# Performance work log

Hardware: AMD Instinct MI355X
Metric: run time of the kernel (lower is better)

## Reference

```python
import jax, jax.numpy as jnp
import numpy as np
from jax import lax

R = 4                      # search_range
FILTERS = [128, 128, 96, 64, 32, 2]
B, H, W, C = 8, 128, 128, 128
IN_CH = (2 * R + 1) ** 2 + C + 2   # 81 + 128 + 2 = 211


def mish(x):
    return x * jnp.tanh(jax.nn.softplus(x))


def sepconv(x, dw, pw, b=None, act=True):
    # depthwise 3x3 (SAME) then pointwise 1x1, matching SeparableConv2D
    cin = x.shape[-1]
    y = lax.conv_general_dilated(
        x, dw, window_strides=(1, 1), padding='SAME',
        dimension_numbers=('NHWC', 'HWIO', 'NHWC'),
        feature_group_count=cin)
    y = jnp.einsum('bhwc,co->bhwo', y, pw)
    if b is not None:
        y = y + b
    return mish(y) if act else y


def warp(img, flo):
    # bilinear backward warp; TF casts float->int32 with truncation, jnp matches
    b_, h, w, _ = img.shape
    xs = jnp.arange(w, dtype=jnp.float32)[None, None, :]
    ys = jnp.arange(h, dtype=jnp.float32)[None, :, None]
    x = xs + flo[..., 0]
    y = ys + flo[..., 1]
    x0 = x.astype(jnp.int32)
    y0 = y.astype(jnp.int32)
    x1 = x0 + 1
    y1 = y0 + 1
    x0c = jnp.clip(x0, 0, w - 1)
    x1c = jnp.clip(x1, 0, w - 1)
    y0c = jnp.clip(y0, 0, h - 1)
    y1c = jnp.clip(y1, 0, h - 1)
    bi = jnp.arange(b_)[:, None, None]
    Ia = img[bi, y0c, x0c]
    Ib = img[bi, y1c, x0c]
    Ic = img[bi, y0c, x1c]
    Id = img[bi, y1c, x1c]
    x0f = x0c.astype(jnp.float32); x1f = x1c.astype(jnp.float32)
    y0f = y0c.astype(jnp.float32); y1f = y1c.astype(jnp.float32)
    wa = ((x1f - x) * (y1f - y))[..., None]
    wb = ((x1f - x) * (y - y0f))[..., None]
    wc = ((x - x0f) * (y1f - y))[..., None]
    wd = ((x - x0f) * (y - y0f))[..., None]
    return wa * Ia + wb * Ib + wc * Ic + wd * Id


def cost_volume(prv, nxt):
    _, h, w, _ = prv.shape
    d = 2 * R + 1
    pad = jnp.pad(nxt, ((0, 0), (R, R), (R, R), (0, 0)))
    costs = [jnp.mean(prv * pad[:, i:i + h, j:j + w, :], axis=-1)
             for i in range(d) for j in range(d)]
    return jnp.stack(costs, axis=-1)  # [B,H,W,81]


def setup_inputs() -> dict:
    key = jax.random.key(0)
    ks = iter(jax.random.split(key, 64))
    inp = {
        'prv': jax.random.normal(next(ks), (B, H, W, C), dtype=jnp.float32),
        'nxt': jax.random.normal(next(ks), (B, H, W, C), dtype=jnp.float32),
        'flo': jax.random.normal(next(ks), (B, H, W, 2), dtype=jnp.float32),
    }
    cin = IN_CH
    for i, f in enumerate(FILTERS):
        inp[f'dw{i}'] = 0.05 * jax.random.normal(next(ks), (3, 3, 1, cin), dtype=jnp.float32)
        inp[f'pw{i}'] = 0.05 * jax.random.normal(next(ks), (cin, f), dtype=jnp.float32)
        if i < len(FILTERS) - 1:
            inp[f'b{i}'] = 0.05 * jax.random.normal(next(ks), (f,), dtype=jnp.float32)
        cin = f
    return inp


def reference(prv, nxt, flo,
              dw0, pw0, b0, dw1, pw1, b1, dw2, pw2, b2,
              dw3, pw3, b3, dw4, pw4, b4, dw5, pw5):
    nxt_w = warp(nxt, flo)
    cost = cost_volume(prv, nxt_w)
    x = jnp.concatenate([cost, prv, flo], axis=-1)  # [B,H,W,211]
    x = sepconv(x, dw0, pw0, b0)
    x = sepconv(x, dw1, pw1, b1)
    x = sepconv(x, dw2, pw2, b2)
    x = sepconv(x, dw3, pw3, b3)
    x = sepconv(x, dw4, pw4, b4)
    x = sepconv(x, dw5, pw5, None, act=False)  # final flow, no bias/activation
    return x
```

## Files before the change

### kernel.cpp

```cpp
#include <hip/hip_runtime.h>
#include <hip/hip_bf16.h>

#define B_ 8
#define H_ 128
#define W_ 128
#define C_ 128

using f32x4 = __attribute__((ext_vector_type(4))) float;
using s16x8 = __attribute__((ext_vector_type(8))) short;
using us4   = __attribute__((ext_vector_type(4))) unsigned short;

__device__ __forceinline__ float mish_f(float x) {
    float t = __expf(fminf(x, 20.0f));
    float u = t * (t + 2.0f);
    return x * u / (u + 2.0f);
}

__device__ __forceinline__ int swz_row(int blk) {
    return ((blk & 7) << 7) | (blk >> 3);
}

__device__ __forceinline__ unsigned short f2bf_rne(float x) {
    unsigned u = __builtin_bit_cast(unsigned, x);
    u += 0x7FFFu + ((u >> 16) & 1u);
    return (unsigned short)(u >> 16);
}
__device__ __forceinline__ float bf2f(unsigned short h) {
    unsigned u = ((unsigned)h) << 16;
    return __builtin_bit_cast(float, u);
}
__device__ __forceinline__ unsigned short f2bf_hw(float x) {
    return __bfloat16_as_ushort(__float2bfloat16(x));
}

__device__ __forceinline__ f32x4 load4u(const float* p) {
    f32x4 v;
    __builtin_memcpy(&v, p, 16);
    return v;
}

__global__ __launch_bounds__(256) void warp_kernel(
    const float* __restrict__ nxt, const float* __restrict__ flo,
    unsigned short* __restrict__ nwh, unsigned short* __restrict__ nwl)
{
    const int tid = threadIdx.x;
    const int c   = tid & 127;
    const int pix = blockIdx.x * 2 + (tid >> 7);
    const int b   = pix >> 14;
    const int rem = pix & 16383;
    const int y   = rem >> 7;
    const int x   = rem & 127;

    const float fx = flo[(size_t)pix * 2 + 0];
    const float fy = flo[(size_t)pix * 2 + 1];
    const float xf = (float)x + fx;
    const float yf = (float)y + fy;
    const int x0 = (int)xf;
    const int y0 = (int)yf;
    const int x0c = min(max(x0, 0), W_ - 1);
    const int x1c = min(max(x0 + 1, 0), W_ - 1);
    const int y0c = min(max(y0, 0), H_ - 1);
    const int y1c = min(max(y0 + 1, 0), H_ - 1);
    const float x0f = (float)x0c, x1f = (float)x1c;
    const float y0f = (float)y0c, y1f = (float)y1c;
    const float wa = (x1f - xf) * (y1f - yf);
    const float wb = (x1f - xf) * (yf - y0f);
    const float wc = (xf - x0f) * (y1f - yf);
    const float wd = (xf - x0f) * (yf - y0f);

    const float* base = nxt + (size_t)b * H_ * W_ * C_;
    const float Ia = base[((size_t)y0c * W_ + x0c) * C_ + c];
    const float Ib = base[((size_t)y1c * W_ + x0c) * C_ + c];
    const float Ic = base[((size_t)y0c * W_ + x1c) * C_ + c];
    const float Id = base[((size_t)y1c * W_ + x1c) * C_ + c];
    const float v  = wa * Ia + wb * Ib + wc * Ic + wd * Id;

    const unsigned short h = f2bf_hw(v);
    const unsigned short l = f2bf_hw(v - bf2f(h));
    nwh[(size_t)pix * C_ + c] = h;
    nwl[(size_t)pix * C_ + c] = l;
}

__global__ __launch_bounds__(1024, 4) void costvol_mfma_kernel(
    const float* __restrict__ prv,
    const unsigned short* __restrict__ nwh,
    const unsigned short* __restrict__ nwl,
    float* __restrict__ cost)
{
    __shared__ __align__(16) unsigned short Nhi[144 * 64];
    __shared__ __align__(16) unsigned short Nlo[144 * 64];
    __shared__ float scr[8][576];

    const int tid  = threadIdx.x;
    const int lane = tid & 63;
    const int wv   = tid >> 6;
    const int w    = wv >> 1;
    const int nt   = wv & 1;
    const int r    = swz_row(blockIdx.x);
    const int y    = r & 127;
    const int b    = r >> 7;
    const int m15  = lane & 15;
    const int kq   = lane >> 4;

    const float* pbase = prv + ((size_t)r * W_ + (w * 16 + m15)) * C_ + kq * 8;
    s16x8 ahi[4], alo[4];
    #pragma unroll
    for (int kt = 0; kt < 4; ++kt) {
        const f32x4 p0 = *(const f32x4*)(pbase + kt * 32);
        const f32x4 p1 = *(const f32x4*)(pbase + kt * 32 + 4);
        #pragma unroll
        for (int j = 0; j < 8; ++j) {
            const float f = (j < 4) ? p0[j] : p1[j - 4];
            const unsigned short hh = f2bf_hw(f);
            ahi[kt][j] = (short)hh;
            alo[kt][j] = (short)f2bf_hw(f - bf2f(hh));
        }
    }

    {
        const int plane = tid >> 9;
        const int rem   = tid & 511;
        const int side  = rem >> 8;
        const int rem2  = rem & 255;
        const int px    = (side ? 136 : 0) + (rem2 >> 5);
        const int dwi   = rem2 & 31;
        unsigned int* dst = (unsigned int*)
            ((plane ? (char*)Nlo : (char*)Nhi) + (size_t)px * 128) + dwi;
        *dst = 0u;
    }
    __syncthreads();

    const int px_mem = (w + nt) * 16 + m15;
    const int swz    = px_mem & 7;
    const int quad   = lane >> 4;

    for (int d = 0; d < 9; ++d) {
        const int q = y + d - 4;
        f32x4 acc = (f32x4){0.f, 0.f, 0.f, 0.f};

        if (q >= 0 && q < H_) {
            const size_t rowb = ((size_t)(b * H_ + q) * W_) * C_;
            #pragma unroll
            for (int kp = 0; kp < 2; ++kp) {
                __syncthreads();
                #pragma unroll
                for (int s = 0; s < 2; ++s) {
                    const int grp   = wv * 2 + s;
                    const int plane = grp >> 4;
                    const int ci    = (grp & 15) * 64 + lane;
                    const int pxi   = ci >> 3;
                    const int slot  = ci & 7;
                    const unsigned short* src =
                        (plane ? nwl : nwh) + rowb
                        + (size_t)pxi * 128 + kp * 64 + slot * 8;
                    const s16x8 v = *(const s16x8*)src;
                    char* bse = plane ? (char*)Nlo : (char*)Nhi;
                    *(s16x8*)(bse + (size_t)(pxi + 8) * 128
                                  + ((slot ^ (pxi & 7)) * 16)) = v;
                }
                __syncthreads();
                #pragma unroll
                for (int j = 0; j < 2; ++j) {
                    const int kt      = kp * 2 + j;
                    const int byteoff = px_mem * 128 + (((j * 4 + kq) ^ swz) * 16);
                    const s16x8 bhi = *(const s16x8*)((const char*)Nhi + byteoff);
                    const s16x8 blo = *(const s16x8*)((const char*)Nlo + byteoff);
                    acc = __builtin_amdgcn_mfma_f32_16x16x32_bf16(alo[kt], bhi, acc, 0, 0, 0);
                    acc = __builtin_amdgcn_mfma_f32_16x16x32_bf16(ahi[kt], blo, acc, 0, 0, 0);
                    acc = __builtin_amdgcn_mfma_f32_16x16x32_bf16(ahi[kt], bhi, acc, 0, 0, 0);
                }
            }
        }

        __syncthreads();
        #pragma unroll
        for (int g = 0; g < 4; ++g)
            scr[w][(quad * 4 + g) * 36 + nt * 16 + m15] = acc[g];
        __syncthreads();
        #pragma unroll
        for (int p = 0; p < 2; ++p) {
            const int local = lane + 64 * p;
            if (local < 72) {
                const int idx = nt * 72 + local;
                const int xl  = idx / 9;
                const int dx  = idx - xl * 9;
                const float v = scr[w][xl * 37 + dx + 4] * (1.0f / 128.0f);
                cost[((size_t)r * W_ + (w * 16 + xl)) * 81 + d * 9 + dx] = v;
            }
        }
    }
}

__global__ __launch_bounds__(256) void prep_kernel(
    const float* __restrict__ pw, int CIN, int COUT, int NT,
    unsigned short* __restrict__ hi, unsigned short* __restrict__ lo)
{
    const int kt = blockIdx.x / NT;
    const int nt = blockIdx.x - kt * NT;
    #pragma unroll
    for (int s = 0; s < 2; ++s) {
        const int e = threadIdx.x + 256 * s;
        const int n = e >> 5, k = e & 31;
        const int kg = kt * 32 + k, ng = nt * 16 + n;
        const float v = (kg < CIN && ng < COUT) ? pw[(size_t)kg * COUT + ng] : 0.0f;
        const unsigned short h = f2bf_rne(v);
        const unsigned short l = f2bf_rne(v - bf2f(h));
        const size_t o = ((size_t)blockIdx.x * 16 + n) * 32 + k;
        hi[o] = h; lo[o] = l;
    }
}

template<int CIN, int COUT, bool ACT, bool IS_L0>
__global__ __launch_bounds__(512, 4) void sepconv_kernel(
    const float* __restrict__ in,
    const float* __restrict__ cost, const float* __restrict__ prv,
    const float* __restrict__ flo,
    const float* __restrict__ dw,
    const unsigned short* __restrict__ Bhi, const unsigned short* __restrict__ Blo,
    const float* __restrict__ bias, float* __restrict__ out)
{
    constexpr int KT   = (CIN + 31) / 32;
    constexpr int KPAD = KT * 32;
    constexpr int NT   = (COUT + 15) / 16;
    constexpr int KSTR = 40;
    __shared__ unsigned short Ahi[128 * KSTR];
    __shared__ unsigned short Alo[128 * KSTR];
    __shared__ float dwl[9 * KPAD];

    const int tid  = threadIdx.x;
    const int lane = tid & 63;
    const int w    = tid >> 6;
    const int r    = swz_row(blockIdx.x);
    const int h    = r & 127;
    const int b    = r >> 7;

    const int co = (tid & 7) * 4;
    const int xb = (tid >> 3) * 2;

    bool rowok[3]; int rowpix[3];
    #pragma unroll
    for (int ky = 0; ky < 3; ++ky) {
        const int yy = h + ky - 1;
        rowok[ky]  = (yy >= 0) && (yy < H_);
        rowpix[ky] = (b * H_ + (rowok[ky] ? yy : h)) * W_;
    }

    for (int i = tid; i < 9 * KPAD; i += 512) {
        const int t = i / KPAD, c = i - t * KPAD;
        dwl[i] = (c < CIN) ? dw[t * CIN + c] : 0.0f;
    }

    f32x4 acc[NT];
    #pragma unroll
    for (int n = 0; n < NT; ++n)
        acc[n] = (f32x4){0.0f, 0.0f, 0.0f, 0.0f};

    __syncthreads();

    for (int kt = 0; kt < KT; ++kt) {
        const int cg = kt * 32 + co;
        f32x4 V[3][4];
        #pragma unroll
        for (int ky = 0; ky < 3; ++ky) {
            #pragma unroll
            for (int xm = 0; xm < 4; ++xm) {
                const int xx = xb - 1 + xm;
                f32x4 v = (f32x4){0.f, 0.f, 0.f, 0.f};
                if (rowok[ky] && xx >= 0 && xx < W_) {
                    const int px = rowpix[ky] + xx;
                    if constexpr (IS_L0) {
                        if (cg <= 76) {
                            v = load4u(cost + (size_t)px * 81 + cg);
                        } else if (cg == 80) {
                            const float* cp = cost + (size_t)px * 81;
                            const float* pp = prv + (size_t)px * 128;
                            v = (f32x4){cp[80], pp[0], pp[1], pp[2]};
                        } else if (cg <= 204) {
                            v = load4u(prv + (size_t)px * 128 + (cg - 81));
                        } else if (cg == 208) {
                            const float* pp = prv + (size_t)px * 128;
                            const float* fp = flo + (size_t)px * 2;
                            v = (f32x4){pp[127], fp[0], fp[1], 0.f};
                        }
                    } else {
                        v = *(const f32x4*)(in + (size_t)px * CIN + cg);
                    }
                }
                V[ky][xm] = v;
            }
        }

        f32x4 a0 = (f32x4){0.f, 0.f, 0.f, 0.f};
        f32x4 a1 = (f32x4){0.f, 0.f, 0.f, 0.f};
        #pragma unroll
        for (int ky = 0; ky < 3; ++ky) {
            #pragma unroll
            for (int kx = 0; kx < 3; ++kx) {
                const f32x4 wv = *(const f32x4*)&dwl[(ky * 3 + kx) * KPAD + cg];
                a0 += wv * V[ky][kx];
                a1 += wv * V[ky][kx + 1];
            }
        }

        us4 h0, l0, h1, l1;
        #pragma unroll
        for (int j = 0; j < 4; ++j) {
            const unsigned short hh0 = f2bf_hw(a0[j]);
            h0[j] = hh0; l0[j] = f2bf_hw(a0[j] - bf2f(hh0));
            const unsigned short hh1 = f2bf_hw(a1[j]);
            h1[j] = hh1; l1[j] = f2bf_hw(a1[j] - bf2f(hh1));
        }

        __syncthreads();
        *(us4*)&Ahi[(xb + 0) * KSTR + co] = h0;
        *(us4*)&Ahi[(xb + 1) * KSTR + co] = h1;
        *(us4*)&Alo[(xb + 0) * KSTR + co] = l0;
        *(us4*)&Alo[(xb + 1) * KSTR + co] = l1;
        __syncthreads();

        const int mrow = w * 16 + (lane & 15);
        const int ko   = (lane >> 4) * 8;
        const s16x8 ahi = *(const s16x8*)&Ahi[mrow * KSTR + ko];
        const s16x8 alo = *(const s16x8*)&Alo[mrow * KSTR + ko];
        #pragma unroll
        for (int nt = 0; nt < NT; ++nt) {
            const size_t boff = (((size_t)(kt * NT + nt)) * 16 + (lane & 15)) * 32
                              + (size_t)ko;
            const s16x8 bhi = *(const s16x8*)&Bhi[boff];
            const s16x8 blo = *(const s16x8*)&Blo[boff];
            acc[nt] = __builtin_amdgcn_mfma_f32_16x16x32_bf16(alo, bhi, acc[nt], 0, 0, 0);
            acc[nt] = __builtin_amdgcn_mfma_f32_16x16x32_bf16(ahi, blo, acc[nt], 0, 0, 0);
            acc[nt] = __builtin_amdgcn_mfma_f32_16x16x32_bf16(ahi, bhi, acc[nt], 0, 0, 0);
        }
    }

    const int n    = lane & 15;
    const int quad = lane >> 4;
    #pragma unroll
    for (int nt = 0; nt < NT; ++nt) {
        const int o = nt * 16 + n;
        if ((COUT % 16 == 0) || (o < COUT)) {
            const float bv = ACT ? bias[o] : 0.0f;
            #pragma unroll
            for (int reg = 0; reg < 4; ++reg) {
                const int px = w * 16 + quad * 4 + reg;
                const float v = acc[nt][reg] + bv;
                out[((size_t)r * W_ + px) * COUT + o] = ACT ? mish_f(v) : v;
            }
        }
    }
}

extern "C" void kernel_launch(void* const* d_in, const int* in_sizes, int n_in,
                              void* d_out, int out_size, void* d_ws, size_t ws_size,
                              hipStream_t stream)
{
    (void)in_sizes; (void)n_in; (void)out_size; (void)ws_size;
    const float* prv = (const float*)d_in[0];
    const float* nxt = (const float*)d_in[1];
    const float* flo = (const float*)d_in[2];
    const float* dw0 = (const float*)d_in[3];
    const float* pw0 = (const float*)d_in[4];
    const float* b0  = (const float*)d_in[5];
    const float* dw1 = (const float*)d_in[6];
    const float* pw1 = (const float*)d_in[7];
    const float* b1  = (const float*)d_in[8];
    const float* dw2 = (const float*)d_in[9];
    const float* pw2 = (const float*)d_in[10];
    const float* b2  = (const float*)d_in[11];
    const float* dw3 = (const float*)d_in[12];
    const float* pw3 = (const float*)d_in[13];
    const float* b3  = (const float*)d_in[14];
    const float* dw4 = (const float*)d_in[15];
    const float* pw4 = (const float*)d_in[16];
    const float* b4  = (const float*)d_in[17];
    const float* dw5 = (const float*)d_in[18];
    const float* pw5 = (const float*)d_in[19];

    char* ws = (char*)d_ws;
    float* bufA = (float*)ws;
    float* bufC = (float*)(ws + 67108864);
    float* costb = bufC;
    float* l4out = (float*)(ws + 67108864 + 33554432);
    float* outp  = (float*)d_out;

    unsigned short* nwh = (unsigned short*)ws;
    unsigned short* nwl = (unsigned short*)(ws + 33554432);

    unsigned short* W0h = (unsigned short*)(ws + 112000000);
    unsigned short* W0l = (unsigned short*)(ws + 112000000 + 57344);
    unsigned short* W1h = (unsigned short*)d_out;
    unsigned short* W1l = (unsigned short*)d_out + 16384;
    unsigned short* W2h = (unsigned short*)(ws + 50331648);
    unsigned short* W2l = (unsigned short*)(ws + 50356224);
    unsigned short* W3h = (unsigned short*)(ws + 50380800);
    unsigned short* W3l = (unsigned short*)(ws + 50393088);
    unsigned short* W4h = (unsigned short*)(ws + 50405376);
    unsigned short* W4l = (unsigned short*)(ws + 50409472);
    unsigned short* W5h = (unsigned short*)(ws + 50413568);
    unsigned short* W5l = (unsigned short*)(ws + 50414592);

    const float* nullf = nullptr;

    warp_kernel<<<65536, 256, 0, stream>>>(nxt, flo, nwh, nwl);
    costvol_mfma_kernel<<<1024, 1024, 0, stream>>>(prv, nwh, nwl, costb);

    prep_kernel<<<7 * 8, 256, 0, stream>>>(pw0, 211, 128, 8, W0h, W0l);
    prep_kernel<<<4 * 8, 256, 0, stream>>>(pw1, 128, 128, 8, W1h, W1l);

    sepconv_kernel<211, 128, true,  true ><<<1024, 512, 0, stream>>>(
        nullf, costb, prv, flo, dw0, W0h, W0l, b0, bufA);
    sepconv_kernel<128, 128, true,  false><<<1024, 512, 0, stream>>>(
        bufA, nullf, nullf, nullf, dw1, W1h, W1l, b1, bufC);

    prep_kernel<<<4 * 6, 256, 0, stream>>>(pw2, 128,  96, 6, W2h, W2l);
    prep_kernel<<<3 * 4, 256, 0, stream>>>(pw3,  96,  64, 4, W3h, W3l);
    prep_kernel<<<2 * 2, 256, 0, stream>>>(pw4,  64,  32, 2, W4h, W4l);
    prep_kernel<<<1 * 1, 256, 0, stream>>>(pw5,  32,   2, 1, W5h, W5l);

    sepconv_kernel<128,  96, true,  false><<<1024, 512, 0, stream>>>(
        bufC, nullf, nullf, nullf, dw2, W2h, W2l, b2, bufA);
    sepconv_kernel< 96,  64, true,  false><<<1024, 512, 0, stream>>>(
        bufA, nullf, nullf, nullf, dw3, W3h, W3l, b3, bufC);
    sepconv_kernel< 64,  32, true,  false><<<1024, 512, 0, stream>>>(
        bufC, nullf, nullf, nullf, dw4, W4h, W4l, b4, l4out);
    sepconv_kernel< 32,   2, false, false><<<1024, 512, 0, stream>>>(
        l4out, nullf, nullf, nullf, dw5, W5h, W5l, nullf, outp);
}
```

Measured before the change: 569.9 us.

## Process two K-tiles per barrier pair with 4-pixel depthwise strips per thread

Result: slower. 1.680 ms (+194.8%).

```diff
diff --git a/kernel.cpp b/kernel.cpp
--- a/kernel.cpp
+++ b/kernel.cpp
@@ -222,7 +222,7 @@
     constexpr int KT   = (CIN + 31) / 32;
     constexpr int KPAD = KT * 32;
     constexpr int NT   = (COUT + 15) / 16;
-    constexpr int KSTR = 40;
+    constexpr int KSTR = 72;
     __shared__ unsigned short Ahi[128 * KSTR];
     __shared__ unsigned short Alo[128 * KSTR];
     __shared__ float dwl[9 * KPAD];
@@ -234,8 +234,10 @@
     const int h    = r & 127;
     const int b    = r >> 7;
 
-    const int co = (tid & 7) * 4;
-    const int xb = (tid >> 3) * 2;
+    const int sub = tid >> 8;
+    const int t   = tid & 255;
+    const int co  = (t & 7) * 4;
+    const int xb  = (t >> 3) * 4;
 
     bool rowok[3]; int rowpix[3];
     #pragma unroll
@@ -246,8 +248,8 @@
     }
 
     for (int i = tid; i < 9 * KPAD; i += 512) {
-        const int t = i / KPAD, c = i - t * KPAD;
-        dwl[i] = (c < CIN) ? dw[t * CIN + c] : 0.0f;
+        const int tt = i / KPAD, c = i - tt * KPAD;
+        dwl[i] = (c < CIN) ? dw[tt * CIN + c] : 0.0f;
     }
 
     f32x4 acc[NT];
@@ -257,80 +259,106 @@
 
     __syncthreads();
 
-    for (int kt = 0; kt < KT; ++kt) {
-        const int cg = kt * 32 + co;
-        f32x4 V[3][4];
-        #pragma unroll
-        for (int ky = 0; ky < 3; ++ky) {
-            #pragma unroll
-            for (int xm = 0; xm < 4; ++xm) {
-                const int xx = xb - 1 + xm;
-                f32x4 v = (f32x4){0.f, 0.f, 0.f, 0.f};
-                if (rowok[ky] && xx >= 0 && xx < W_) {
-                    const int px = rowpix[ky] + xx;
-                    if constexpr (IS_L0) {
-                        if (cg <= 76) {
-                            v = load4u(cost + (size_t)px * 81 + cg);
-                        } else if (cg == 80) {
-                            const float* cp = cost + (size_t)px * 81;
-                            const float* pp = prv + (size_t)px * 128;
-                            v = (f32x4){cp[80], pp[0], pp[1], pp[2]};
-                        } else if (cg <= 204) {
-                            v = load4u(prv + (size_t)px * 128 + (cg - 81));
-                        } else if (cg == 208) {
-                            const float* pp = prv + (size_t)px * 128;
-                            const float* fp = flo + (size_t)px * 2;
-                            v = (f32x4){pp[127], fp[0], fp[1], 0.f};
-                        }
-                    } else {
-                        v = *(const f32x4*)(in + (size_t)px * CIN + cg);
+    const int mrow = w * 16 + (lane & 15);
+    const int kq8  = (lane >> 4) * 8;
+
+    for (int kt0 = 0; kt0 < KT; kt0 += 2) {
+        const int  kt     = kt0 + sub;
+        const bool active = (kt < KT);
+        const int  cg     = kt * 32 + co;
+
+        f32x4 a[4];
+        #pragma unroll
+        for (int i = 0; i < 4; ++i) a[i] = (f32x4){0.f, 0.f, 0.f, 0.f};
+
+        if (active) {
+            auto ldpx = [&](int px) -> f32x4 {
+                if constexpr (IS_L0) {
+                    if (cg <= 76) {
+                        return load4u(cost + (size_t)px * 81 + cg);
+                    } else if (cg == 80) {
+                        const float* cp = cost + (size_t)px * 81;
+                        const float* pp = prv + (size_t)px * 128;
+                        return (f32x4){cp[80], pp[0], pp[1], pp[2]};
+                    } else if (cg <= 204) {
+                        return load4u(prv + (size_t)px * 128 + (cg - 81));
+                    } else if (cg == 208) {
+                        const float* pp = prv + (size_t)px * 128;
+                        const float* fp = flo + (size_t)px * 2;
+                        return (f32x4){pp[127], fp[0], fp[1], 0.f};
+                    }
+                    return (f32x4){0.f, 0.f, 0.f, 0.f};
+                } else {
+                    return *(const f32x4*)(in + (size_t)px * CIN + cg);
+                }
+            };
+
+            #pragma unroll
+            for (int ky = 0; ky < 3; ++ky) {
+                f32x4 wk0 = (f32x4){0.f,0.f,0.f,0.f};
+                f32x4 wk1 = wk0, wk2 = wk0;
+                if (rowok[ky]) {
+                    wk0 = *(const f32x4*)&dwl[(ky * 3 + 0) * KPAD + cg];
+                    wk1 = *(const f32x4*)&dwl[(ky * 3 + 1) * KPAD + cg];
+                    wk2 = *(const f32x4*)&dwl[(ky * 3 + 2) * KPAD + cg];
+                }
+                f32x4 v[6];
+                if (xb != 0 && xb != 124) {
+                    #pragma unroll
+                    for (int m = 0; m < 6; ++m)
+                        v[m] = ldpx(rowpix[ky] + xb - 1 + m);
+                } else {
+                    #pragma unroll
+                    for (int m = 0; m < 6; ++m) {
+                        const int xs = xb - 1 + m;
+                        const bool ok = (xs >= 0) && (xs < W_);
+                        v[m] = ok ? ldpx(rowpix[ky] + xs)
+                                  : (f32x4){0.f, 0.f, 0.f, 0.f};
                     }
                 }
-                V[ky][xm] = v;
-            }
-        }
-
-        f32x4 a0 = (f32x4){0.f, 0.f, 0.f, 0.f};
-        f32x4 a1 = (f32x4){0.f, 0.f, 0.f, 0.f};
-        #pragma unroll
-        for (int ky = 0; ky < 3; ++ky) {
-            #pragma unroll
-            for (int kx = 0; kx < 3; ++kx) {
-                const f32x4 wv = *(const f32x4*)&dwl[(ky * 3 + kx) * KPAD + cg];
-                a0 += wv * V[ky][kx];
-                a1 += wv * V[ky][kx + 1];
-            }
-        }
-
-        us4 h0, l0, h1, l1;
-        #pragma unroll
-        for (int j = 0; j < 4; ++j) {
-            const unsigned short hh0 = f2bf_hw(a0[j]);
-            h0[j] = hh0; l0[j] = f2bf_hw(a0[j] - bf2f(hh0));
-            const unsigned short hh1 = f2bf_hw(a1[j]);
-            h1[j] = hh1; l1[j] = f2bf_hw(a1[j] - bf2f(hh1));
+                #pragma unroll
+                for (int i = 0; i < 4; ++i)
+                    a[i] += wk0 * v[i] + wk1 * v[i + 1] + wk2 * v[i + 2];
+            }
+        }
+
+        us4 hh[4], ll[4];
+        #pragma unroll
+        for (int i = 0; i < 4; ++i) {
+            #pragma unroll
+            for (int j = 0; j < 4; ++j) {
+                const unsigned short hv = f2bf_hw(a[i][j]);
+                hh[i][j] = hv;
+                ll[i][j] = f2bf_hw(a[i][j] - bf2f(hv));
+            }
         }
 
         __syncthreads();
-        *(us4*)&Ahi[(xb + 0) * KSTR + co] = h0;
-        *(us4*)&Ahi[(xb + 1) * KSTR + co] = h1;
-        *(us4*)&Alo[(xb + 0) * KSTR + co] = l0;
-        *(us4*)&Alo[(xb + 1) * KSTR + co] = l1;
+        if (active) {
+            #pragma unroll
+            for (int i = 0; i < 4; ++i) {
+                *(us4*)&Ahi[(xb + i) * KSTR + sub * 32 + co] = hh[i];
+                *(us4*)&Alo[(xb + i) * KSTR + sub * 32 + co] = ll[i];
+            }
+        }
         __syncthreads();
 
-        const int mrow = w * 16 + (lane & 15);
-        const int ko   = (lane >> 4) * 8;
-        const s16x8 ahi = *(const s16x8*)&Ahi[mrow * KSTR + ko];
-        const s16x8 alo = *(const s16x8*)&Alo[mrow * KSTR + ko];
-        #pragma unroll
-        for (int nt = 0; nt < NT; ++nt) {
-            const size_t boff = (((size_t)(kt * NT + nt)) * 16 + (lane & 15)) * 32
-                              + (size_t)ko;
-            const s16x8 bhi = *(const s16x8*)&Bhi[boff];
-            const s16x8 blo = *(const s16x8*)&Blo[boff];
-            acc[nt] = __builtin_amdgcn_mfma_f32_16x16x32_bf16(alo, bhi, acc[nt], 0, 0, 0);
-            acc[nt] = __builtin_amdgcn_mfma_f32_16x16x32_bf16(ahi, blo, acc[nt], 0, 0, 0);
-            acc[nt] = __builtin_amdgcn_mfma_f32_16x16x32_bf16(ahi, bhi, acc[nt], 0, 0, 0);
+        #pragma unroll
+        for (int s2 = 0; s2 < 2; ++s2) {
+            if (kt0 + s2 >= KT) break;
+            const s16x8 ahi = *(const s16x8*)&Ahi[mrow * KSTR + s2 * 32 + kq8];
+            const s16x8 alo = *(const s16x8*)&Alo[mrow * KSTR + s2 * 32 + kq8];
+            #pragma unroll
+            for (int nt = 0; nt < NT; ++nt) {
+                const size_t boff =
+                    (((size_t)((kt0 + s2) * NT + nt)) * 16 + (lane & 15)) * 32
+                    + (size_t)kq8;
+                const s16x8 bhi = *(const s16x8*)&Bhi[boff];
+                const s16x8 blo = *(const s16x8*)&Blo[boff];
+                acc[nt] = __builtin_amdgcn_mfma_f32_16x16x32_bf16(alo, bhi, acc[nt], 0, 0, 0);
+                acc[nt] = __builtin_amdgcn_mfma_f32_16x16x32_bf16(ahi, blo, acc[nt], 0, 0, 0);
+                acc[nt] = __builtin_amdgcn_mfma_f32_16x16x32_bf16(ahi, bhi, acc[nt], 0, 0, 0);
+            }
         }
     }
 
```

## Stage depthwise input halo tile in shared memory before 3x3 conv

Applied to the files above, without the earlier changes.

New measurement: 608.1 us. 1.07x slower.

```diff
diff --git a/kernel.cpp b/kernel.cpp
--- a/kernel.cpp
+++ b/kernel.cpp
@@ -223,9 +223,10 @@
     constexpr int KPAD = KT * 32;
     constexpr int NT   = (COUT + 15) / 16;
     constexpr int KSTR = 40;
-    __shared__ unsigned short Ahi[128 * KSTR];
-    __shared__ unsigned short Alo[128 * KSTR];
+    __shared__ __align__(16) float INb[3 * 130 * 32];
     __shared__ float dwl[9 * KPAD];
+    unsigned short* Ahi = (unsigned short*)INb;
+    unsigned short* Alo = (unsigned short*)INb + 5120;
 
     const int tid  = threadIdx.x;
     const int lane = tid & 63;
@@ -257,49 +258,65 @@
 
     __syncthreads();
 
+    const int mrow = w * 16 + (lane & 15);
+    const int kq8  = (lane >> 4) * 8;
+
     for (int kt = 0; kt < KT; ++kt) {
-        const int cg = kt * 32 + co;
-        f32x4 V[3][4];
-        #pragma unroll
-        for (int ky = 0; ky < 3; ++ky) {
-            #pragma unroll
-            for (int xm = 0; xm < 4; ++xm) {
-                const int xx = xb - 1 + xm;
+        __syncthreads();
+
+        const int cgb = kt * 32;
+        #pragma unroll
+        for (int i = 0; i < 7; ++i) {
+            const int idx = tid + 512 * i;
+            if (idx < 3120) {
+                const int ky  = idx / 1040;
+                const int rem = idx - ky * 1040;
+                const int px  = rem >> 3;
+                const int c4  = (rem & 7) * 4;
                 f32x4 v = (f32x4){0.f, 0.f, 0.f, 0.f};
-                if (rowok[ky] && xx >= 0 && xx < W_) {
-                    const int px = rowpix[ky] + xx;
+                if (px >= 1 && px <= 128) {
+                    const int pxg = rowpix[ky] + (px - 1);
+                    const int cg  = cgb + c4;
                     if constexpr (IS_L0) {
                         if (cg <= 76) {
-                            v = load4u(cost + (size_t)px * 81 + cg);
+                            v = load4u(cost + (size_t)pxg * 81 + cg);
                         } else if (cg == 80) {
-                            const float* cp = cost + (size_t)px * 81;
-                            const float* pp = prv + (size_t)px * 128;
+                            const float* cp = cost + (size_t)pxg * 81;
+                            const float* pp = prv + (size_t)pxg * 128;
                             v = (f32x4){cp[80], pp[0], pp[1], pp[2]};
                         } else if (cg <= 204) {
-                            v = load4u(prv + (size_t)px * 128 + (cg - 81));
+                            v = load4u(prv + (size_t)pxg * 128 + (cg - 81));
                         } else if (cg == 208) {
-                            const float* pp = prv + (size_t)px * 128;
-                            const float* fp = flo + (size_t)px * 2;
+                            const float* pp = prv + (size_t)pxg * 128;
+                            const float* fp = flo + (size_t)pxg * 2;
                             v = (f32x4){pp[127], fp[0], fp[1], 0.f};
                         }
                     } else {
-                        v = *(const f32x4*)(in + (size_t)px * CIN + cg);
+                        v = *(const f32x4*)(in + (size_t)pxg * CIN + cg);
                     }
                 }
-                V[ky][xm] = v;
+                *(f32x4*)&INb[(size_t)idx * 4] = v;
             }
         }
+        __syncthreads();
 
         f32x4 a0 = (f32x4){0.f, 0.f, 0.f, 0.f};
         f32x4 a1 = (f32x4){0.f, 0.f, 0.f, 0.f};
         #pragma unroll
         for (int ky = 0; ky < 3; ++ky) {
-            #pragma unroll
-            for (int kx = 0; kx < 3; ++kx) {
-                const f32x4 wv = *(const f32x4*)&dwl[(ky * 3 + kx) * KPAD + cg];
-                a0 += wv * V[ky][kx];
-                a1 += wv * V[ky][kx + 1];
+            f32x4 w0 = (f32x4){0.f,0.f,0.f,0.f}, w1 = w0, w2 = w0;
+            if (rowok[ky]) {
+                w0 = *(const f32x4*)&dwl[(ky * 3 + 0) * KPAD + cgb + co];
+                w1 = *(const f32x4*)&dwl[(ky * 3 + 1) * KPAD + cgb + co];
+                w2 = *(const f32x4*)&dwl[(ky * 3 + 2) * KPAD + cgb + co];
             }
+            const float* bp = &INb[(ky * 130 + xb) * 32 + co];
+            const f32x4 v0 = *(const f32x4*)(bp);
+            const f32x4 v1 = *(const f32x4*)(bp + 32);
+            const f32x4 v2 = *(const f32x4*)(bp + 64);
+            const f32x4 v3 = *(const f32x4*)(bp + 96);
+            a0 += w0 * v0 + w1 * v1 + w2 * v2;
+            a1 += w0 * v1 + w1 * v2 + w2 * v3;
         }
 
         us4 h0, l0, h1, l1;
@@ -318,14 +335,12 @@
         *(us4*)&Alo[(xb + 1) * KSTR + co] = l1;
         __syncthreads();
 
-        const int mrow = w * 16 + (lane & 15);
-        const int ko   = (lane >> 4) * 8;
-        const s16x8 ahi = *(const s16x8*)&Ahi[mrow * KSTR + ko];
-        const s16x8 alo = *(const s16x8*)&Alo[mrow * KSTR + ko];
+        const s16x8 ahi = *(const s16x8*)&Ahi[mrow * KSTR + kq8];
+        const s16x8 alo = *(const s16x8*)&Alo[mrow * KSTR + kq8];
         #pragma unroll
         for (int nt = 0; nt < NT; ++nt) {
             const size_t boff = (((size_t)(kt * NT + nt)) * 16 + (lane & 15)) * 32
-                              + (size_t)ko;
+                              + (size_t)kq8;
             const s16x8 bhi = *(const s16x8*)&Bhi[boff];
             const s16x8 blo = *(const s16x8*)&Blo[boff];
             acc[nt] = __builtin_amdgcn_mfma_f32_16x16x32_bf16(alo, bhi, acc[nt], 0, 0, 0);
```
